# Optimization experiments

Hardware: AMD Instinct MI355X
Metric: run time of the kernel (lower is better)

## Reference

```python
import jax, jax.numpy as jnp
import numpy as np

T, B, D, H, L = 512, 128, 256, 256, 4


def setup_inputs() -> dict:
    key = jax.random.key(0)
    ks = jax.random.split(key, 12)
    s = 0.05  # weight scale for stable gating
    lengths = jnp.sort(jax.random.randint(ks[1], (B,), 1, T + 1))[::-1].astype(jnp.int32)
    return {
        "x": jax.random.normal(ks[0], (T, B, D), jnp.float32),
        "lengths": lengths,  # sorted descending, as in a PackedSequence
        "Wr": jax.random.normal(ks[2], (D + H, H), jnp.float32) * s,
        "Wz": jax.random.normal(ks[3], (D + H, H), jnp.float32) * s,
        "Wl": jax.random.normal(ks[4], (D + H, H), jnp.float32) * s,
        "Wt": jax.random.normal(ks[5], (D, H), jnp.float32) * s,
        "Cx": jax.random.normal(ks[6], (D, H), jnp.float32) * s,
        "Ch": jax.random.normal(ks[7], (H, H), jnp.float32) * s,
        "Tr": jax.random.normal(ks[8], (L, H, H), jnp.float32) * s,
        "Tz": jax.random.normal(ks[9], (L, H, H), jnp.float32) * s,
        "Tn": jax.random.normal(ks[10], (L, H, H), jnp.float32) * s,
    }


def _cell(xt, h, Wr, Wz, Wl, Wt, Cx, Ch, Tr, Tz, Tn):
    # LinearEnchancedGRU
    cat = jnp.concatenate([xt, h], axis=-1)  # [B, D+H]
    r = jax.nn.sigmoid(cat @ Wr)
    z = jax.nn.sigmoid(cat @ Wz)
    l = jax.nn.sigmoid(cat @ Wl)
    n = jnp.tanh(xt @ Cx + r * (h @ Ch)) + l * (xt @ Wt)
    h = (1.0 - z) * h + z * n
    # stack of TransitionGRU cells (fixed small depth)
    for i in range(Tr.shape[0]):
        rr = jax.nn.sigmoid(h @ Tr[i])
        zz = jax.nn.sigmoid(h @ Tz[i])
        nn_ = jnp.tanh(rr * (h @ Tn[i]))
        h = (1.0 - zz) * nn_ + zz * h
    return h


def reference(x, lengths, Wr, Wz, Wl, Wt, Cx, Ch, Tr, Tz, Tn):
    # Packed-sequence semantics: at step t only the first batchSizes[t] rows are
    # active (lengths sorted descending => mask[t] = t < lengths). Inactive rows
    # keep their old hidden (equivalent to hx[:batch] truncation) and emit 0
    # (row absent from the packed output).
    Tn_steps, Bn, _ = x.shape
    Hn = Ch.shape[0]
    mask = jnp.arange(Tn_steps)[:, None] < lengths[None, :]  # [T, B]

    def step(h, inp):
        xt, m = inp
        hn = _cell(xt, h, Wr, Wz, Wl, Wt, Cx, Ch, Tr, Tz, Tn)
        m = m[:, None]
        h = jnp.where(m, hn, h)
        out = jnp.where(m, hn, jnp.zeros_like(hn))
        return h, out

    h0 = jnp.zeros((Bn, Hn), x.dtype)
    _, outs = jax.lax.scan(step, h0, (x, mask))
    return outs  # [T, B, H], zero-padded beyond each sequence's length
```

## Files before the change

### kernel.cpp

```cpp
#include <hip/hip_runtime.h>
#include <hip/hip_bf16.h>
#include <string.h>

#define T_STEPS 512
#define BATCH   128
#define DIM     256
#define HID     256
#define NLAYERS 4

typedef unsigned int  uint4v  __attribute__((ext_vector_type(4)));
typedef unsigned int  uint2v  __attribute__((ext_vector_type(2)));
typedef short         short8  __attribute__((ext_vector_type(8)));
typedef float         float4v __attribute__((ext_vector_type(4)));

#define SLOT_BYTES  (128 * 1024)
#define NSLOTS      4
#define HBUF_BYTES  (NSLOTS * SLOT_BYTES)

__device__ __forceinline__ short8 as_s8(uint4v u) {
  union { uint4v u; short8 s; } x; x.u = u; return x.s;
}
__device__ __forceinline__ float sigf(float x) {
  return 1.0f / (1.0f + __expf(-x));
}
__device__ __forceinline__ float tanh_fast(float x) {
  x = fminf(fmaxf(x, -15.0f), 15.0f);
  float e = __expf(2.0f * x);
  return (e - 1.0f) / (e + 1.0f);
}
__device__ __forceinline__ unsigned short f2bf(float a) {
  unsigned ua = __builtin_bit_cast(unsigned, a);
  return (unsigned short)((ua + 0x7FFFu + ((ua >> 16) & 1u)) >> 16);
}
__device__ __forceinline__ unsigned pack_bf16x2(float a, float b) {
  return (unsigned)f2bf(a) | ((unsigned)f2bf(b) << 16);
}
__device__ __forceinline__ uint4v extract_frag(uint4v a, uint4v b) {
  uint4v f; f.x = a.x; f.y = a.z; f.z = b.x; f.w = b.z; return f;
}
__device__ __forceinline__ unsigned tagbad(uint4v a, uint4v b, unsigned tag) {
  return (a.y ^ tag) | (a.w ^ tag) | (b.y ^ tag) | (b.w ^ tag);
}

#define GLD16(A0,B0,A1,B1,A2,B2,A3,B3,A4,B4,A5,B5,A6,B6,A7,B7, ADDR)       \
  asm volatile(                                                             \
      "global_load_dwordx4 %0, %16, off offset:0 sc0 sc1\n\t"               \
      "global_load_dwordx4 %1, %16, off offset:16 sc0 sc1\n\t"              \
      "global_load_dwordx4 %2, %16, off offset:128 sc0 sc1\n\t"             \
      "global_load_dwordx4 %3, %16, off offset:144 sc0 sc1\n\t"             \
      "global_load_dwordx4 %4, %16, off offset:256 sc0 sc1\n\t"             \
      "global_load_dwordx4 %5, %16, off offset:272 sc0 sc1\n\t"             \
      "global_load_dwordx4 %6, %16, off offset:384 sc0 sc1\n\t"             \
      "global_load_dwordx4 %7, %16, off offset:400 sc0 sc1\n\t"             \
      "global_load_dwordx4 %8, %16, off offset:512 sc0 sc1\n\t"             \
      "global_load_dwordx4 %9, %16, off offset:528 sc0 sc1\n\t"             \
      "global_load_dwordx4 %10, %16, off offset:640 sc0 sc1\n\t"            \
      "global_load_dwordx4 %11, %16, off offset:656 sc0 sc1\n\t"            \
      "global_load_dwordx4 %12, %16, off offset:768 sc0 sc1\n\t"            \
      "global_load_dwordx4 %13, %16, off offset:784 sc0 sc1\n\t"            \
      "global_load_dwordx4 %14, %16, off offset:896 sc0 sc1\n\t"            \
      "global_load_dwordx4 %15, %16, off offset:912 sc0 sc1\n\t"            \
      "s_waitcnt vmcnt(0)"                                                  \
      : "=&v"(A0), "=&v"(B0), "=&v"(A1), "=&v"(B1),                         \
        "=&v"(A2), "=&v"(B2), "=&v"(A3), "=&v"(B3),                         \
        "=&v"(A4), "=&v"(B4), "=&v"(A5), "=&v"(B5),                         \
        "=&v"(A6), "=&v"(B6), "=&v"(A7), "=&v"(B7)                          \
      : "v"(ADDR)                                                           \
      : "memory")

#define POLL8T(F0,F1,F2,F3,F4,F5,F6,F7, ADDR, TAG)                          \
  {                                                                         \
    uint4v _a0,_b0,_a1,_b1,_a2,_b2,_a3,_b3,_a4,_b4,_a5,_b5,_a6,_b6,_a7,_b7; \
    for (int _it = 0;; ++_it) {                                             \
      GLD16(_a0,_b0,_a1,_b1,_a2,_b2,_a3,_b3,_a4,_b4,_a5,_b5,_a6,_b6,_a7,_b7,\
            ADDR);                                                          \
      unsigned _bad = tagbad(_a0,_b0,TAG) | tagbad(_a1,_b1,TAG) |           \
                      tagbad(_a2,_b2,TAG) | tagbad(_a3,_b3,TAG) |           \
                      tagbad(_a4,_b4,TAG) | tagbad(_a5,_b5,TAG) |           \
                      tagbad(_a6,_b6,TAG) | tagbad(_a7,_b7,TAG);            \
      if (__all((int)(_bad == 0u)) || _it > (1 << 16)) break;               \
      if (_it >= 16) __builtin_amdgcn_s_sleep(1);                           \
    }                                                                       \
    F0 = extract_frag(_a0,_b0); F1 = extract_frag(_a1,_b1);                 \
    F2 = extract_frag(_a2,_b2); F3 = extract_frag(_a3,_b3);                 \
    F4 = extract_frag(_a4,_b4); F5 = extract_frag(_a5,_b5);                 \
    F6 = extract_frag(_a6,_b6); F7 = extract_frag(_a7,_b7);                 \
  }

#define PUBLISH(ADDR, PACKED, TAG)                                          \
  {                                                                         \
    uint2v _pv; _pv.x = (PACKED); _pv.y = (TAG);                            \
    asm volatile("global_store_dwordx2 %0, %1, off sc0 sc1"                 \
                 :: "v"(ADDR), "v"(_pv) : "memory");                        \
  }

#define DRAIN_STORES                                                        \
  { asm volatile("s_waitcnt vmcnt(0)" ::: "memory"); }

#define MFMA_K8_2(AX, AY, BARR, H0,H1,H2,H3,H4,H5,H6,H7)                             \
  AX = __builtin_amdgcn_mfma_f32_16x16x32_bf16(as_s8(H0), BARR[0], AX, 0, 0, 0);     \
  AY = __builtin_amdgcn_mfma_f32_16x16x32_bf16(as_s8(H1), BARR[1], AY, 0, 0, 0);     \
  AX = __builtin_amdgcn_mfma_f32_16x16x32_bf16(as_s8(H2), BARR[2], AX, 0, 0, 0);     \
  AY = __builtin_amdgcn_mfma_f32_16x16x32_bf16(as_s8(H3), BARR[3], AY, 0, 0, 0);     \
  AX = __builtin_amdgcn_mfma_f32_16x16x32_bf16(as_s8(H4), BARR[4], AX, 0, 0, 0);     \
  AY = __builtin_amdgcn_mfma_f32_16x16x32_bf16(as_s8(H5), BARR[5], AY, 0, 0, 0);     \
  AX = __builtin_amdgcn_mfma_f32_16x16x32_bf16(as_s8(H6), BARR[6], AX, 0, 0, 0);     \
  AY = __builtin_amdgcn_mfma_f32_16x16x32_bf16(as_s8(H7), BARR[7], AY, 0, 0, 0);

__launch_bounds__(256, 1)
__global__ void rnn_main(const float* __restrict__ x,
                         const int* __restrict__ lengths,
                         const float* __restrict__ Wr,
                         const float* __restrict__ Wz,
                         const float* __restrict__ Wl,
                         const float* __restrict__ Wt,
                         const float* __restrict__ Cx,
                         const float* __restrict__ Ch,
                         const float* __restrict__ Tr,
                         const float* __restrict__ Tz,
                         const float* __restrict__ Tn,
                         unsigned char* __restrict__ hbuf,
                         float* __restrict__ out) {
  const int tid  = threadIdx.x;
  const int lane = tid & 63;
  const int v    = tid >> 6;
  const int bid  = blockIdx.x;
  const int c    = bid & 7;
  const int w    = bid >> 3;

  __shared__ float  tiles[6][16 * 20];
  __shared__ uint4v hsh[8][64];
  __shared__ uint4v xsh[8][64];
  __shared__ int    len_sh[16];

  short8 Wf[6][8];
  {
    const int SCHED[4][6] = {{0, 4, 9, 10, 11, 12},
                             {1, 5, 13, 14, 15, 16},
                             {2, 6, 17, 18, 19, 20},
                             {3, 7, 8, 3, 3, 3}};
    const int colg = w * 16 + (lane & 15);
#pragma unroll
    for (int s = 0; s < 6; ++s) {
      const int m = SCHED[v][s];
      const float* base;
      int ro = 0;
      if      (m == 0)  { base = Wr; ro = 256; }
      else if (m == 1)  { base = Wz; ro = 256; }
      else if (m == 2)  { base = Wl; ro = 256; }
      else if (m == 3)  { base = Ch; }
      else if (m == 4)  { base = Wr; }
      else if (m == 5)  { base = Wz; }
      else if (m == 6)  { base = Wl; }
      else if (m == 7)  { base = Cx; }
      else if (m == 8)  { base = Wt; }
      else if (m <= 12) { base = Tr + (size_t)(m - 9)  * HID * HID; }
      else if (m <= 16) { base = Tz + (size_t)(m - 13) * HID * HID; }
      else              { base = Tn + (size_t)(m - 17) * HID * HID; }
#pragma unroll
      for (int kt = 0; kt < 8; ++kt) {
        const int k0 = ro + kt * 32 + (lane >> 4) * 8;
        short8 f;
#pragma unroll
        for (int j = 0; j < 8; ++j)
          f[j] = (short)f2bf(base[(size_t)(k0 + j) * HID + colg]);
        Wf[s][kt] = f;
      }
    }
  }

  if (tid < 16) len_sh[tid] = lengths[c * 16 + tid];

  const float* xbase =
      x + ((size_t)c * 16 + (lane & 15)) * DIM + (lane >> 4) * 8;

  if (v == 1) {
#pragma unroll
    for (int kt = 0; kt < 8; ++kt) {
      float4v xa = *(const float4v*)(xbase + kt * 32);
      float4v xb = *(const float4v*)(xbase + kt * 32 + 4);
      uint4v f;
      f.x = pack_bf16x2(xa.x, xa.y);
      f.y = pack_bf16x2(xa.z, xa.w);
      f.z = pack_bf16x2(xb.x, xb.y);
      f.w = pack_bf16x2(xb.z, xb.w);
      xsh[kt][lane] = f;
    }
  }
  __syncthreads();

  const int row = tid >> 4;
  const int col = tid & 15;
  const int mylen = len_sh[row];
  const int ci = col * 20 + row;

  float hreg = 0.0f, hprev = 0.0f;

  const unsigned vh = (unsigned)((c * 16 + (lane & 15)) * 1024 + (lane >> 4) * 32);
  const unsigned pub_off =
      (unsigned)(((c * 16 + (tid >> 4)) * 128 + w * 8 + ((tid & 15) >> 1)) * 8);

  for (int t = 0; t < T_STEPS; ++t) {
    const int r0 = t * 5;
    float4v xra[8], xrb[8];
    {
      uint4v xf[8];
#pragma unroll
      for (int kt = 0; kt < 8; ++kt) xf[kt] = xsh[kt][lane];

      float4v a0 = {0.f, 0.f, 0.f, 0.f};
      float4v a1 = {0.f, 0.f, 0.f, 0.f};
      float4v a2 = {0.f, 0.f, 0.f, 0.f};
      if (v < 3) {
#pragma unroll
        for (int kt = 0; kt < 8; ++kt)
          a0 = __builtin_amdgcn_mfma_f32_16x16x32_bf16(as_s8(xf[kt]), Wf[1][kt], a0, 0, 0, 0);
      } else {
#pragma unroll
        for (int kt = 0; kt < 8; ++kt)
          a1 = __builtin_amdgcn_mfma_f32_16x16x32_bf16(as_s8(xf[kt]), Wf[1][kt], a1, 0, 0, 0);
#pragma unroll
        for (int kt = 0; kt < 8; ++kt)
          a2 = __builtin_amdgcn_mfma_f32_16x16x32_bf16(as_s8(xf[kt]), Wf[2][kt], a2, 0, 0, 0);
      }
      uint4v h0, h1, h2, h3, h4, h5, h6, h7;
      if (v == 0) {
        const unsigned char* ap =
            hbuf + (size_t)((r0 - 1) & 3) * SLOT_BYTES + vh;
        POLL8T(h0, h1, h2, h3, h4, h5, h6, h7, ap, (unsigned)r0);
        hsh[0][lane] = h0; hsh[1][lane] = h1; hsh[2][lane] = h2;
        hsh[3][lane] = h3; hsh[4][lane] = h4; hsh[5][lane] = h5;
        hsh[6][lane] = h6; hsh[7][lane] = h7;
      }
      __syncthreads();
      if (v != 0) {
        h0 = hsh[0][lane]; h1 = hsh[1][lane]; h2 = hsh[2][lane];
        h3 = hsh[3][lane]; h4 = hsh[4][lane]; h5 = hsh[5][lane];
        h6 = hsh[6][lane]; h7 = hsh[7][lane];
      }
      {
        float4v ahx = {0.f, 0.f, 0.f, 0.f};
        float4v ahy = {0.f, 0.f, 0.f, 0.f};
        MFMA_K8_2(ahx, ahy, Wf[0], h0, h1, h2, h3, h4, h5, h6, h7);
        a0 = a0 + ahx + ahy;
      }
      {
        float* tp = &tiles[(v < 3) ? v : 3][(lane & 15) * 20 + (lane >> 4) * 4];
        *(float4v*)tp = a0;
        if (v == 3) {
          *(float4v*)&tiles[4][(lane & 15) * 20 + (lane >> 4) * 4] = a1;
          *(float4v*)&tiles[5][(lane & 15) * 20 + (lane >> 4) * 4] = a2;
        }
      }
      __syncthreads();
      float rp  = tiles[0][ci], zp = tiles[1][ci], lp = tiles[2][ci];
      float chv = tiles[3][ci], xcv = tiles[4][ci], xwv = tiles[5][ci];
      float r  = sigf(rp), z = sigf(zp), lg = sigf(lp);
      float n  = tanh_fast(xcv + r * chv) + lg * xwv;
      hreg = (1.0f - z) * hreg + z * n;
      {
        float hp = __shfl_xor(hreg, 1);
        if (!(tid & 1)) {
          unsigned char* pp = hbuf + (size_t)(r0 & 3) * SLOT_BYTES + pub_off;
          PUBLISH(pp, pack_bf16x2(hreg, hp), (unsigned)(r0 + 1));
        }
        if (v != 0) DRAIN_STORES;
      }
    }
#pragma unroll
    for (int i = 0; i < NLAYERS; ++i) {
      const int ri = r0 + 1 + i;
      if (v == 1 && t + 1 < T_STEPS) {
        if (i == 0) {
          const float* xq = xbase + (size_t)(t + 1) * BATCH * DIM;
#pragma unroll
          for (int kt = 0; kt < 8; ++kt) {
            xra[kt] = *(const float4v*)(xq + kt * 32);
            xrb[kt] = *(const float4v*)(xq + kt * 32 + 4);
          }
        }
        if (i == 1) {
#pragma unroll
          for (int kt = 0; kt < 8; ++kt) {
            uint4v f;
            f.x = pack_bf16x2(xra[kt].x, xra[kt].y);
            f.y = pack_bf16x2(xra[kt].z, xra[kt].w);
            f.z = pack_bf16x2(xrb[kt].x, xrb[kt].y);
            f.w = pack_bf16x2(xrb[kt].z, xrb[kt].w);
            xsh[kt][lane] = f;
          }
        }
      }
      uint4v h0, h1, h2, h3, h4, h5, h6, h7;
      if (v == 0) {
        const unsigned char* ap =
            hbuf + (size_t)((ri - 1) & 3) * SLOT_BYTES + vh;
        POLL8T(h0, h1, h2, h3, h4, h5, h6, h7, ap, (unsigned)ri);
        hsh[0][lane] = h0; hsh[1][lane] = h1; hsh[2][lane] = h2;
        hsh[3][lane] = h3; hsh[4][lane] = h4; hsh[5][lane] = h5;
        hsh[6][lane] = h6; hsh[7][lane] = h7;
      }
      __syncthreads();
      if (v < 3) {
        if (v != 0) {
          h0 = hsh[0][lane]; h1 = hsh[1][lane]; h2 = hsh[2][lane];
          h3 = hsh[3][lane]; h4 = hsh[4][lane]; h5 = hsh[5][lane];
          h6 = hsh[6][lane]; h7 = hsh[7][lane];
        }
        float4v ahx = {0.f, 0.f, 0.f, 0.f};
        float4v ahy = {0.f, 0.f, 0.f, 0.f};
        MFMA_K8_2(ahx, ahy, Wf[2 + i], h0, h1, h2, h3, h4, h5, h6, h7);
        ahx = ahx + ahy;
        *(float4v*)&tiles[v][(lane & 15) * 20 + (lane >> 4) * 4] = ahx;
      }
      __syncthreads();
      float rr = sigf(tiles[0][ci]);
      float zz = sigf(tiles[1][ci]);
      float nn = tanh_fast(rr * tiles[2][ci]);
      hreg = (1.0f - zz) * nn + zz * hreg;
      if (i == NLAYERS - 1) {
        const bool act = (t < mylen);
        float hv = act ? hreg : hprev;
        float ov = act ? hreg : 0.0f;
        hreg = hv;
        hprev = hv;
        out[((size_t)t * BATCH + c * 16 + row) * HID + w * 16 + col] = ov;
      }
      {
        float hp = __shfl_xor(hreg, 1);
        if (!(tid & 1)) {
          unsigned char* pp = hbuf + (size_t)(ri & 3) * SLOT_BYTES + pub_off;
          PUBLISH(pp, pack_bf16x2(hreg, hp), (unsigned)(ri + 1));
        }
        if (v != 0) DRAIN_STORES;
      }
    }
  }
}

extern "C" void kernel_launch(void* const* d_in, const int* in_sizes, int n_in,
                              void* d_out, int out_size, void* d_ws, size_t ws_size,
                              hipStream_t stream) {
  (void)in_sizes; (void)n_in; (void)out_size; (void)ws_size;
  const float* x        = (const float*)d_in[0];
  const int* lengths    = (const int*)d_in[1];
  const float* Wr       = (const float*)d_in[2];
  const float* Wz       = (const float*)d_in[3];
  const float* Wl       = (const float*)d_in[4];
  const float* Wt       = (const float*)d_in[5];
  const float* Cx       = (const float*)d_in[6];
  const float* Ch       = (const float*)d_in[7];
  const float* Tr       = (const float*)d_in[8];
  const float* Tz       = (const float*)d_in[9];
  const float* Tn       = (const float*)d_in[10];

  unsigned char* hbuf = (unsigned char*)d_ws;

  hipMemsetAsync(hbuf, 0x00, HBUF_BYTES, stream);

  rnn_main<<<dim3(128), dim3(256), 0, stream>>>(
      x, lengths, Wr, Wz, Wl, Wt, Cx, Ch, Tr, Tz, Tn,
      hbuf, (float*)d_out);
}
```

Before: 7.571 ms.

## Replace block barriers with LDS flag handshakes and centralize gate combine in wave 0

Replaces the two __syncthreads per sub-step with LDS acquire/release flags. Wave 0 polls the global hidden state, writes it to shared memory, raises a flag and waits on a counter; waves 1-3 compute the r/z/n gate MFMAs and signal completion. The gate combine and the global publish now happen only in wave 0, with each lane handling four rows, so the per-wave store drains are gone. This shortens the synchronization chain on the serial recurrence, at the cost of spin-wait overhead and more elementwise work concentrated in one wave.

After: 8.830 ms. 1.17x slower.

```diff
diff --git a/kernel.cpp b/kernel.cpp
--- a/kernel.cpp
+++ b/kernel.cpp
@@ -40,6 +40,22 @@
 }
 __device__ __forceinline__ unsigned tagbad(uint4v a, uint4v b, unsigned tag) {
   return (a.y ^ tag) | (a.w ^ tag) | (b.y ^ tag) | (b.w ^ tag);
+}
+
+__device__ __forceinline__ unsigned ldacq(unsigned* p) {
+  return __hip_atomic_load(p, __ATOMIC_ACQUIRE, __HIP_MEMORY_SCOPE_WORKGROUP);
+}
+__device__ __forceinline__ void strel(unsigned* p, unsigned val) {
+  __hip_atomic_store(p, val, __ATOMIC_RELEASE, __HIP_MEMORY_SCOPE_WORKGROUP);
+}
+__device__ __forceinline__ void addrel(unsigned* p) {
+  __hip_atomic_fetch_add(p, 1u, __ATOMIC_RELEASE, __HIP_MEMORY_SCOPE_WORKGROUP);
+}
+__device__ __forceinline__ void waitflag(unsigned* p, unsigned tgt) {
+  int it = 0;
+  while (ldacq(p) < tgt) {
+    if (++it > 512) __builtin_amdgcn_s_sleep(1);
+  }
 }
 
 #define GLD16(A0,B0,A1,B1,A2,B2,A3,B3,A4,B4,A5,B5,A6,B6,A7,B7, ADDR)       \
@@ -94,18 +110,8 @@
                  :: "v"(ADDR), "v"(_pv) : "memory");                        \
   }
 
-#define DRAIN_STORES                                                        \
-  { asm volatile("s_waitcnt vmcnt(0)" ::: "memory"); }
-
-#define MFMA_K8_2(AX, AY, BARR, H0,H1,H2,H3,H4,H5,H6,H7)                             \
-  AX = __builtin_amdgcn_mfma_f32_16x16x32_bf16(as_s8(H0), BARR[0], AX, 0, 0, 0);     \
-  AY = __builtin_amdgcn_mfma_f32_16x16x32_bf16(as_s8(H1), BARR[1], AY, 0, 0, 0);     \
-  AX = __builtin_amdgcn_mfma_f32_16x16x32_bf16(as_s8(H2), BARR[2], AX, 0, 0, 0);     \
-  AY = __builtin_amdgcn_mfma_f32_16x16x32_bf16(as_s8(H3), BARR[3], AY, 0, 0, 0);     \
-  AX = __builtin_amdgcn_mfma_f32_16x16x32_bf16(as_s8(H4), BARR[4], AX, 0, 0, 0);     \
-  AY = __builtin_amdgcn_mfma_f32_16x16x32_bf16(as_s8(H5), BARR[5], AY, 0, 0, 0);     \
-  AX = __builtin_amdgcn_mfma_f32_16x16x32_bf16(as_s8(H6), BARR[6], AX, 0, 0, 0);     \
-  AY = __builtin_amdgcn_mfma_f32_16x16x32_bf16(as_s8(H7), BARR[7], AY, 0, 0, 0);
+#define MFMA1(ACC, HF, BF)                                                  \
+  ACC = __builtin_amdgcn_mfma_f32_16x16x32_bf16(as_s8(HF), BF, ACC, 0, 0, 0)
 
 __launch_bounds__(256, 1)
 __global__ void rnn_main(const float* __restrict__ x,
@@ -128,17 +134,18 @@
   const int c    = bid & 7;
   const int w    = bid >> 3;
 
-  __shared__ float  tiles[6][16 * 20];
-  __shared__ uint4v hsh[8][64];
-  __shared__ uint4v xsh[8][64];
-  __shared__ int    len_sh[16];
+  __shared__ float    tiles[3][256];
+  __shared__ uint4v   hsh[8][64];
+  __shared__ uint4v   xsh[8][64];
+  __shared__ unsigned hsflag;
+  __shared__ unsigned tcnt;
 
   short8 Wf[6][8];
   {
-    const int SCHED[4][6] = {{0, 4, 9, 10, 11, 12},
+    const int SCHED[4][6] = {{3, 7, 8, 3, 3, 3},
+                             {0, 4, 9, 10, 11, 12},
                              {1, 5, 13, 14, 15, 16},
-                             {2, 6, 17, 18, 19, 20},
-                             {3, 7, 8, 3, 3, 3}};
+                             {2, 6, 17, 18, 19, 20}};
     const int colg = w * 16 + (lane & 15);
 #pragma unroll
     for (int s = 0; s < 6; ++s) {
@@ -169,7 +176,21 @@
     }
   }
 
-  if (tid < 16) len_sh[tid] = lengths[c * 16 + tid];
+  if (tid == 0) { hsflag = 0u; tcnt = 0u; }
+
+  const int rb  = (lane >> 4) * 4;
+  const int col = lane & 15;
+
+  int   len4[4];
+  float h_state[4], hfroz[4];
+  if (v == 0) {
+#pragma unroll
+    for (int j = 0; j < 4; ++j) {
+      len4[j]    = lengths[c * 16 + rb + j];
+      h_state[j] = 0.0f;
+      hfroz[j]   = 0.0f;
+    }
+  }
 
   const float* xbase =
       x + ((size_t)c * 16 + (lane & 15)) * DIM + (lane >> 4) * 8;
@@ -189,150 +210,177 @@
   }
   __syncthreads();
 
-  const int row = tid >> 4;
-  const int col = tid & 15;
-  const int mylen = len_sh[row];
-  const int ci = col * 20 + row;
-
-  float hreg = 0.0f, hprev = 0.0f;
-
   const unsigned vh = (unsigned)((c * 16 + (lane & 15)) * 1024 + (lane >> 4) * 32);
-  const unsigned pub_off =
-      (unsigned)(((c * 16 + (tid >> 4)) * 128 + w * 8 + ((tid & 15) >> 1)) * 8);
+  const unsigned pub0 =
+      (unsigned)(((c * 16 + rb) * 128 + w * 8 + (col >> 1)) * 8);
+
+  unsigned exp_cnt = 0;
 
   for (int t = 0; t < T_STEPS; ++t) {
     const int r0 = t * 5;
-    float4v xra[8], xrb[8];
+    float4v xra[8], xrb8[8];
     {
       uint4v xf[8];
 #pragma unroll
       for (int kt = 0; kt < 8; ++kt) xf[kt] = xsh[kt][lane];
 
-      float4v a0 = {0.f, 0.f, 0.f, 0.f};
-      float4v a1 = {0.f, 0.f, 0.f, 0.f};
-      float4v a2 = {0.f, 0.f, 0.f, 0.f};
-      if (v < 3) {
-#pragma unroll
-        for (int kt = 0; kt < 8; ++kt)
-          a0 = __builtin_amdgcn_mfma_f32_16x16x32_bf16(as_s8(xf[kt]), Wf[1][kt], a0, 0, 0, 0);
-      } else {
-#pragma unroll
-        for (int kt = 0; kt < 8; ++kt)
-          a1 = __builtin_amdgcn_mfma_f32_16x16x32_bf16(as_s8(xf[kt]), Wf[1][kt], a1, 0, 0, 0);
-#pragma unroll
-        for (int kt = 0; kt < 8; ++kt)
-          a2 = __builtin_amdgcn_mfma_f32_16x16x32_bf16(as_s8(xf[kt]), Wf[2][kt], a2, 0, 0, 0);
-      }
-      uint4v h0, h1, h2, h3, h4, h5, h6, h7;
       if (v == 0) {
+        float4v acx = {0.f,0.f,0.f,0.f}, awt = {0.f,0.f,0.f,0.f};
+#pragma unroll
+        for (int kt = 0; kt < 8; ++kt) {
+          MFMA1(acx, xf[kt], Wf[1][kt]);
+          MFMA1(awt, xf[kt], Wf[2][kt]);
+        }
+        uint4v hf[8];
         const unsigned char* ap =
             hbuf + (size_t)((r0 - 1) & 3) * SLOT_BYTES + vh;
-        POLL8T(h0, h1, h2, h3, h4, h5, h6, h7, ap, (unsigned)r0);
-        hsh[0][lane] = h0; hsh[1][lane] = h1; hsh[2][lane] = h2;
-        hsh[3][lane] = h3; hsh[4][lane] = h4; hsh[5][lane] = h5;
-        hsh[6][lane] = h6; hsh[7][lane] = h7;
-      }
-      __syncthreads();
-      if (v != 0) {
-        h0 = hsh[0][lane]; h1 = hsh[1][lane]; h2 = hsh[2][lane];
-        h3 = hsh[3][lane]; h4 = hsh[4][lane]; h5 = hsh[5][lane];
-        h6 = hsh[6][lane]; h7 = hsh[7][lane];
-      }
-      {
-        float4v ahx = {0.f, 0.f, 0.f, 0.f};
-        float4v ahy = {0.f, 0.f, 0.f, 0.f};
-        MFMA_K8_2(ahx, ahy, Wf[0], h0, h1, h2, h3, h4, h5, h6, h7);
-        a0 = a0 + ahx + ahy;
-      }
-      {
-        float* tp = &tiles[(v < 3) ? v : 3][(lane & 15) * 20 + (lane >> 4) * 4];
-        *(float4v*)tp = a0;
-        if (v == 3) {
-          *(float4v*)&tiles[4][(lane & 15) * 20 + (lane >> 4) * 4] = a1;
-          *(float4v*)&tiles[5][(lane & 15) * 20 + (lane >> 4) * 4] = a2;
-        }
-      }
-      __syncthreads();
-      float rp  = tiles[0][ci], zp = tiles[1][ci], lp = tiles[2][ci];
-      float chv = tiles[3][ci], xcv = tiles[4][ci], xwv = tiles[5][ci];
-      float r  = sigf(rp), z = sigf(zp), lg = sigf(lp);
-      float n  = tanh_fast(xcv + r * chv) + lg * xwv;
-      hreg = (1.0f - z) * hreg + z * n;
-      {
-        float hp = __shfl_xor(hreg, 1);
-        if (!(tid & 1)) {
-          unsigned char* pp = hbuf + (size_t)(r0 & 3) * SLOT_BYTES + pub_off;
-          PUBLISH(pp, pack_bf16x2(hreg, hp), (unsigned)(r0 + 1));
-        }
-        if (v != 0) DRAIN_STORES;
+        POLL8T(hf[0],hf[1],hf[2],hf[3],hf[4],hf[5],hf[6],hf[7],
+               ap, (unsigned)r0);
+#pragma unroll
+        for (int k = 0; k < 8; ++k) hsh[k][lane] = hf[k];
+        if (lane == 0) strel(&hsflag, (unsigned)(r0 + 1));
+        float4v c1 = {0.f,0.f,0.f,0.f}, c2 = {0.f,0.f,0.f,0.f};
+#pragma unroll
+        for (int kt = 0; kt < 8; kt += 2) {
+          MFMA1(c1, hf[kt],     Wf[0][kt]);
+          MFMA1(c2, hf[kt + 1], Wf[0][kt + 1]);
+        }
+        float4v ach = c1 + c2;
+        exp_cnt += 3;
+        waitflag(&tcnt, exp_cnt);
+        float hnew[4];
+#pragma unroll
+        for (int j = 0; j < 4; ++j) {
+          float r  = tiles[0][lane * 4 + j];
+          float z  = tiles[1][lane * 4 + j];
+          float lg = tiles[2][lane * 4 + j];
+          float n  = tanh_fast(acx[j] + r * ach[j]) + lg * awt[j];
+          hnew[j]  = (1.0f - z) * h_state[j] + z * n;
+          h_state[j] = hnew[j];
+        }
+        float hp0 = __shfl_xor(hnew[0], 1), hp1 = __shfl_xor(hnew[1], 1),
+              hp2 = __shfl_xor(hnew[2], 1), hp3 = __shfl_xor(hnew[3], 1);
+        if (!(lane & 1)) {
+          unsigned char* pp = hbuf + (size_t)(r0 & 3) * SLOT_BYTES + pub0;
+          PUBLISH(pp,        pack_bf16x2(hnew[0], hp0), (unsigned)(r0 + 1));
+          PUBLISH(pp + 1024, pack_bf16x2(hnew[1], hp1), (unsigned)(r0 + 1));
+          PUBLISH(pp + 2048, pack_bf16x2(hnew[2], hp2), (unsigned)(r0 + 1));
+          PUBLISH(pp + 3072, pack_bf16x2(hnew[3], hp3), (unsigned)(r0 + 1));
+        }
+      } else {
+        float4v a1 = {0.f,0.f,0.f,0.f}, a2 = {0.f,0.f,0.f,0.f};
+#pragma unroll
+        for (int kt = 0; kt < 8; kt += 2) {
+          MFMA1(a1, xf[kt],     Wf[1][kt]);
+          MFMA1(a2, xf[kt + 1], Wf[1][kt + 1]);
+        }
+        waitflag(&hsflag, (unsigned)(r0 + 1));
+        uint4v hf[8];
+#pragma unroll
+        for (int k = 0; k < 8; ++k) hf[k] = hsh[k][lane];
+#pragma unroll
+        for (int kt = 0; kt < 8; kt += 2) {
+          MFMA1(a1, hf[kt],     Wf[0][kt]);
+          MFMA1(a2, hf[kt + 1], Wf[0][kt + 1]);
+        }
+        float4v a = a1 + a2;
+#pragma unroll
+        for (int j = 0; j < 4; ++j) a[j] = sigf(a[j]);
+        *(float4v*)&tiles[v - 1][lane * 4] = a;
+        if (lane == 0) addrel(&tcnt);
       }
     }
 #pragma unroll
     for (int i = 0; i < NLAYERS; ++i) {
       const int ri = r0 + 1 + i;
-      if (v == 1 && t + 1 < T_STEPS) {
-        if (i == 0) {
-          const float* xq = xbase + (size_t)(t + 1) * BATCH * DIM;
-#pragma unroll
-          for (int kt = 0; kt < 8; ++kt) {
-            xra[kt] = *(const float4v*)(xq + kt * 32);
-            xrb[kt] = *(const float4v*)(xq + kt * 32 + 4);
-          }
-        }
-        if (i == 1) {
-#pragma unroll
-          for (int kt = 0; kt < 8; ++kt) {
-            uint4v f;
-            f.x = pack_bf16x2(xra[kt].x, xra[kt].y);
-            f.y = pack_bf16x2(xra[kt].z, xra[kt].w);
-            f.z = pack_bf16x2(xrb[kt].x, xrb[kt].y);
-            f.w = pack_bf16x2(xrb[kt].z, xrb[kt].w);
-            xsh[kt][lane] = f;
-          }
-        }
-      }
-      uint4v h0, h1, h2, h3, h4, h5, h6, h7;
       if (v == 0) {
+        uint4v hf[8];
         const unsigned char* ap =
             hbuf + (size_t)((ri - 1) & 3) * SLOT_BYTES + vh;
-        POLL8T(h0, h1, h2, h3, h4, h5, h6, h7, ap, (unsigned)ri);
-        hsh[0][lane] = h0; hsh[1][lane] = h1; hsh[2][lane] = h2;
-        hsh[3][lane] = h3; hsh[4][lane] = h4; hsh[5][lane] = h5;
-        hsh[6][lane] = h6; hsh[7][lane] = h7;
-      }
-      __syncthreads();
-      if (v < 3) {
-        if (v != 0) {
-          h0 = hsh[0][lane]; h1 = hsh[1][lane]; h2 = hsh[2][lane];
-          h3 = hsh[3][lane]; h4 = hsh[4][lane]; h5 = hsh[5][lane];
-          h6 = hsh[6][lane]; h7 = hsh[7][lane];
-        }
-        float4v ahx = {0.f, 0.f, 0.f, 0.f};
-        float4v ahy = {0.f, 0.f, 0.f, 0.f};
-        MFMA_K8_2(ahx, ahy, Wf[2 + i], h0, h1, h2, h3, h4, h5, h6, h7);
-        ahx = ahx + ahy;
-        *(float4v*)&tiles[v][(lane & 15) * 20 + (lane >> 4) * 4] = ahx;
-      }
-      __syncthreads();
-      float rr = sigf(tiles[0][ci]);
-      float zz = sigf(tiles[1][ci]);
-      float nn = tanh_fast(rr * tiles[2][ci]);
-      hreg = (1.0f - zz) * nn + zz * hreg;
-      if (i == NLAYERS - 1) {
-        const bool act = (t < mylen);
-        float hv = act ? hreg : hprev;
-        float ov = act ? hreg : 0.0f;
-        hreg = hv;
-        hprev = hv;
-        out[((size_t)t * BATCH + c * 16 + row) * HID + w * 16 + col] = ov;
-      }
-      {
-        float hp = __shfl_xor(hreg, 1);
-        if (!(tid & 1)) {
-          unsigned char* pp = hbuf + (size_t)(ri & 3) * SLOT_BYTES + pub_off;
-          PUBLISH(pp, pack_bf16x2(hreg, hp), (unsigned)(ri + 1));
-        }
-        if (v != 0) DRAIN_STORES;
+        POLL8T(hf[0],hf[1],hf[2],hf[3],hf[4],hf[5],hf[6],hf[7],
+               ap, (unsigned)ri);
+#pragma unroll
+        for (int k = 0; k < 8; ++k) hsh[k][lane] = hf[k];
+        if (lane == 0) strel(&hsflag, (unsigned)(ri + 1));
+        exp_cnt += 3;
+        waitflag(&tcnt, exp_cnt);
+        float hnew[4];
+        bool  act4[4];
+#pragma unroll
+        for (int j = 0; j < 4; ++j) {
+          float rr = tiles[0][lane * 4 + j];
+          float zz = tiles[1][lane * 4 + j];
+          float tn = tiles[2][lane * 4 + j];
+          float nn = tanh_fast(rr * tn);
+          hnew[j]  = (1.0f - zz) * nn + zz * h_state[j];
+          act4[j]  = true;
+        }
+        if (i == NLAYERS - 1) {
+#pragma unroll
+          for (int j = 0; j < 4; ++j) {
+            act4[j] = (t < len4[j]);
+            float hv = act4[j] ? hnew[j] : hfroz[j];
+            hnew[j]  = hv;
+            hfroz[j] = hv;
+          }
+        }
+#pragma unroll
+        for (int j = 0; j < 4; ++j) h_state[j] = hnew[j];
+        float hp0 = __shfl_xor(hnew[0], 1), hp1 = __shfl_xor(hnew[1], 1),
+              hp2 = __shfl_xor(hnew[2], 1), hp3 = __shfl_xor(hnew[3], 1);
+        if (!(lane & 1)) {
+          unsigned char* pp = hbuf + (size_t)(ri & 3) * SLOT_BYTES + pub0;
+          PUBLISH(pp,        pack_bf16x2(hnew[0], hp0), (unsigned)(ri + 1));
+          PUBLISH(pp + 1024, pack_bf16x2(hnew[1], hp1), (unsigned)(ri + 1));
+          PUBLISH(pp + 2048, pack_bf16x2(hnew[2], hp2), (unsigned)(ri + 1));
+          PUBLISH(pp + 3072, pack_bf16x2(hnew[3], hp3), (unsigned)(ri + 1));
+        }
+        if (i == NLAYERS - 1) {
+#pragma unroll
+          for (int j = 0; j < 4; ++j) {
+            float ov = act4[j] ? hnew[j] : 0.0f;
+            out[((size_t)t * BATCH + c * 16 + rb + j) * HID + w * 16 + col] = ov;
+          }
+        }
+      } else {
+        if (v == 1 && t + 1 < T_STEPS) {
+          if (i == 0) {
+            const float* xq = xbase + (size_t)(t + 1) * BATCH * DIM;
+#pragma unroll
+            for (int kt = 0; kt < 8; ++kt) {
+              xra[kt]  = *(const float4v*)(xq + kt * 32);
+              xrb8[kt] = *(const float4v*)(xq + kt * 32 + 4);
+            }
+          }
+          if (i == 1) {
+#pragma unroll
+            for (int kt = 0; kt < 8; ++kt) {
+              uint4v f;
+              f.x = pack_bf16x2(xra[kt].x, xra[kt].y);
+              f.y = pack_bf16x2(xra[kt].z, xra[kt].w);
+              f.z = pack_bf16x2(xrb8[kt].x, xrb8[kt].y);
+              f.w = pack_bf16x2(xrb8[kt].z, xrb8[kt].w);
+              xsh[kt][lane] = f;
+            }
+          }
+        }
+        waitflag(&hsflag, (unsigned)(ri + 1));
+        uint4v hf[8];
+#pragma unroll
+        for (int k = 0; k < 8; ++k) hf[k] = hsh[k][lane];
+        float4v a1 = {0.f,0.f,0.f,0.f}, a2 = {0.f,0.f,0.f,0.f};
+#pragma unroll
+        for (int kt = 0; kt < 8; kt += 2) {
+          MFMA1(a1, hf[kt],     Wf[2 + i][kt]);
+          MFMA1(a2, hf[kt + 1], Wf[2 + i][kt + 1]);
+        }
+        float4v a = a1 + a2;
+        if (v < 3) {
+#pragma unroll
+          for (int j = 0; j < 4; ++j) a[j] = sigf(a[j]);
+        }
+        *(float4v*)&tiles[v - 1][lane * 4] = a;
+        if (lane == 0) addrel(&tcnt);
       }
     }
   }
```
